# Kernel optimization log

Measured on AMD Instinct MI355X. Metric: run time of the kernel, lower is better.

The kernel has to match this reference:

```python
import jax, jax.numpy as jnp
import numpy as np

D = 300      # dim_in (hardcoded in HGConv)
N_CAT = 3    # n_categories
M = 16384    # nodes
E = 4096     # hyperedges


def setup_inputs() -> dict:
    key = jax.random.key(0)
    ks = jax.random.split(key, 11)
    s = 1.0 / np.sqrt(D)
    u = lambda k, shape: jax.random.uniform(k, shape, jnp.float32, -s, s)
    return {
        "node_feats": jax.random.normal(ks[0], (M, D), jnp.float32),
        "edge_feats": jax.random.normal(ks[1], (E, D), jnp.float32),
        "inc_mat": jax.random.uniform(ks[2], (M, E), jnp.float32),
        # VertexConv params (Linear weights stored as (in, out); torch stores transpose)
        "W_att": u(ks[3], (D, D)),       # attention, no bias
        "W_proj": u(ks[4], (D, D)),      # projection, no bias
        "alpha": jnp.array(0.5, jnp.float32),
        # HypergraphEdgeAggregation params
        "ec_W_att": u(ks[5], (D, 1)),    # attention, no bias
        "ec_W_proj": u(ks[6], (D, D)),
        "ec_b_proj": u(ks[7], (D,)),
        # final classifier
        "fc_W": u(ks[8], (D, N_CAT)),
        "fc_b": u(ks[9], (N_CAT,)),
    }


def reference(node_feats, edge_feats, inc_mat, W_att, W_proj, alpha,
              ec_W_att, ec_W_proj, ec_b_proj, fc_W, fc_b):
    # --- VertexConv ---
    # edge attention scores: inc^T @ (X @ W_att)  -> (e, d)
    edge_att = inc_mat.T @ (node_feats @ W_att)
    attn = jax.nn.softmax(edge_att, axis=1)
    # fused equivalent of einsum('me,md->med') then einsum('med,ed->ed'):
    # edge_feat[e,d] = (inc^T @ X)[e,d] * attn[e,d]
    ef = (inc_mat.T @ node_feats) * attn
    ef = ef @ W_proj
    ef = alpha * edge_feats + (1.0 - alpha) * ef          # residual mix
    # --- HypergraphEdgeAggregation ---
    scores = ef @ ec_W_att                                # (e, 1)
    w = jax.nn.softmax(scores, axis=0)                    # softmax over edges
    pooled = jnp.sum(ef * w, axis=0)                      # (d,)
    out = pooled @ ec_W_proj + ec_b_proj                  # (d,)
    # --- classifier (LogSoftmax is defined but NOT applied in forward) ---
    logits = out @ fc_W + fc_b                            # (n_categories,)
    return logits
```

## Files before the change

kernel.cpp:

```cpp
#include <hip/hip_runtime.h>
#include <math.h>

typedef _Float16 f16;
typedef _Float16 f16x8 __attribute__((ext_vector_type(8)));
typedef _Float16 f16x4 __attribute__((ext_vector_type(4)));
typedef __fp16 fp16x2 __attribute__((ext_vector_type(2)));
typedef float f32x4 __attribute__((ext_vector_type(4)));
typedef float f32x16 __attribute__((ext_vector_type(16)));

#define NM 16384
#define NE 4096
#define ND 300
#define DP 320
#define JT 640
#define PS 2621440

__device__ __forceinline__ int swz(int r) { return (r ^ (r >> 2)) & 3; }

#define GLOAD_LDS16(gsrc, ldst)                                              \
  __builtin_amdgcn_global_load_lds(                                          \
      (__attribute__((address_space(1))) void*)(gsrc),                       \
      (__attribute__((address_space(3))) void*)(ldst), 16, 0, 0)

__global__ void k0_wt(const float* __restrict__ Watt, f16* __restrict__ WT) {
  int idx = blockIdx.x * 256 + threadIdx.x;
  if (idx >= DP * DP) return;
  int j = idx / DP, d = idx % DP;
  float v = (j < ND && d < ND) ? Watt[d * ND + j] : 0.f;
  WT[(size_t)j * DP + d] = (f16)v;
}

__global__ __launch_bounds__(256) void k1a_xprep(const float* __restrict__ X,
                                                 f16* __restrict__ X16,
                                                 f16* __restrict__ YT) {
  __shared__ f16 tile[64][324];
  int m0 = blockIdx.x * 64;
  for (int idx = threadIdx.x; idx < 64 * 80; idx += 256) {
    int m = idx / 80, q = idx % 80;
    int d = q * 4;
    float4 v = make_float4(0.f, 0.f, 0.f, 0.f);
    if (d < ND) v = *(const float4*)(X + (size_t)(m0 + m) * ND + d);
    f16x4 hv;
    hv[0] = (f16)v.x; hv[1] = (f16)v.y; hv[2] = (f16)v.z; hv[3] = (f16)v.w;
    tile[m][d] = hv[0]; tile[m][d + 1] = hv[1];
    tile[m][d + 2] = hv[2]; tile[m][d + 3] = hv[3];
    *(f16x4*)(X16 + (size_t)(m0 + m) * DP + d) = hv;
  }
  __syncthreads();
  for (int idx = threadIdx.x; idx < DP * 8; idx += 256) {
    int d = idx >> 3, part = idx & 7;
    f16x8 hv;
#pragma unroll
    for (int i = 0; i < 8; ++i) hv[i] = tile[part * 8 + i][d];
    *(f16x8*)(YT + (size_t)(DP + d) * NM + m0 + part * 8) = hv;
  }
}

__global__ __launch_bounds__(512, 2) void k1b_xat(const f16* __restrict__ WT,
                                                  const f16* __restrict__ X16,
                                                  f16* __restrict__ YT) {
  __shared__ __align__(16) char lds[49152];
  const int t = threadIdx.x, lane = t & 63, wid = t >> 6;
  const int m0 = blockIdx.x * 64;
  const int row = lane & 15, g = lane >> 4;
  const int wj = wid & 3, wm = wid >> 2;
  int aoff[5], boff[2];
#pragma unroll
  for (int f = 0; f < 5; ++f) {
    int jr = wj * 80 + f * 16 + row;
    aoff[f] = jr * 64 + ((g ^ swz(jr)) << 4);
  }
#pragma unroll
  for (int fm = 0; fm < 2; ++fm) {
    int mr = wm * 32 + fm * 16 + row;
    boff[fm] = mr * 64 + ((g ^ swz(mr)) << 4);
  }
  f32x4 acc[5][2];
#pragma unroll
  for (int f = 0; f < 5; ++f)
#pragma unroll
    for (int fm = 0; fm < 2; ++fm)
#pragma unroll
      for (int r = 0; r < 4; ++r) acc[f][fm][r] = 0.f;

  auto stage = [&](int buf, int ks) {
    int k0 = ks * 32;
    char* A = lds + buf * 20480;
    char* B = lds + 40960 + buf * 4096;
    for (int c = wid; c < 24; c += 8) {
      if (c < 20) {
        int j = c * 16 + (lane >> 2), gg = lane & 3;
        GLOAD_LDS16(WT + (size_t)j * DP + k0 + 8 * (gg ^ swz(j)), A + c * 1024);
      } else {
        int cb = c - 20;
        int m = cb * 16 + (lane >> 2), gg = lane & 3;
        GLOAD_LDS16(X16 + (size_t)(m0 + m) * DP + k0 + 8 * (gg ^ swz(m)),
                    B + cb * 1024);
      }
    }
  };
  stage(0, 0);
  __syncthreads();
  for (int ks = 0; ks < 10; ++ks) {
    int cur = ks & 1;
    if (ks + 1 < 10) stage(cur ^ 1, ks + 1);
    const char* A = lds + cur * 20480;
    const char* B = lds + 40960 + cur * 4096;
    f16x8 b0 = *(const f16x8*)(B + boff[0]);
    f16x8 b1 = *(const f16x8*)(B + boff[1]);
#pragma unroll
    for (int f = 0; f < 5; ++f) {
      f16x8 a = *(const f16x8*)(A + aoff[f]);
      acc[f][0] = __builtin_amdgcn_mfma_f32_16x16x32_f16(a, b0, acc[f][0], 0, 0, 0);
      acc[f][1] = __builtin_amdgcn_mfma_f32_16x16x32_f16(a, b1, acc[f][1], 0, 0, 0);
    }
    __syncthreads();
  }
#pragma unroll
  for (int f = 0; f < 5; ++f)
#pragma unroll
    for (int fm = 0; fm < 2; ++fm)
#pragma unroll
      for (int r = 0; r < 4; ++r) {
        int j = wj * 80 + f * 16 + g * 4 + r;
        int m = m0 + wm * 32 + fm * 16 + row;
        YT[(size_t)j * NM + m] = (f16)acc[f][fm][r];
      }
}

#define K2WAIT(N) asm volatile("s_waitcnt vmcnt(" #N ") lgkmcnt(0)" ::: "memory")
#define K2BAR()                                        \
  do {                                                 \
    asm volatile("" ::: "memory");                     \
    __builtin_amdgcn_s_barrier();                      \
    asm volatile("" ::: "memory");                     \
  } while (0)

__global__ __launch_bounds__(256, 2) void k2_bigmm(const float* __restrict__ inc,
                                                   const f16* __restrict__ YT,
                                                   f16* __restrict__ Zp) {
  constexpr int STEPS = 64;
  __shared__ __align__(16) char lds[57344];
  const int t = threadIdx.x, lane = t & 63, wid = t >> 6;
  const int bx = blockIdx.x;
  const int kb = bx & 7, y = bx >> 3;
  const int eb = y & 31, jn = y >> 5;
  const int e0 = eb * 128, j0 = jn * 320;
  const size_t kbase = (size_t)kb * 2048;
  f16* __restrict__ Zout = Zp + (size_t)kb * PS;

  const int we = wid >> 1, wj = wid & 1;
  const int l31 = lane & 31, oct = lane >> 5;
  int sl[2];
#pragma unroll
  for (int kk = 0; kk < 2; ++kk)
    sl[kk] = (((kk * 2 + oct) ^ ((l31 >> 1) & 3)) & 3) << 4;
  const int arow = (we * 64 + l31) * 64;
  const int brow = (wj * 160 + l31) * 64;
  const int ep = t & 63, kq = t >> 6;
  const int sA = (kq ^ ((ep >> 1) & 3)) & 3;
  const int wa0 = 40960 + ep * 64 + sA * 16;
  const int wa1 = 40960 + (ep + 64) * 64 + sA * 16;
  const float* pA = inc + (kbase + kq * 8) * NE + e0 + ep;
  const int br = wid * 80 + (lane >> 2);
  const f16* pB = YT + (size_t)(j0 + br) * NM + kbase +
                  8 * ((lane & 3) ^ ((lane >> 3) & 3));

  float rAx[8], rAy[8], rBx[8], rBy[8];
  f32x16 acc[2][5];
#pragma unroll
  for (int me = 0; me < 2; ++me)
#pragma unroll
    for (int f = 0; f < 5; ++f)
#pragma unroll
      for (int r = 0; r < 16; ++r) acc[me][f][r] = 0.f;

#define LOADA(RX, RY)                                                          \
  {                                                                            \
    _Pragma("unroll") for (int i = 0; i < 8; ++i) {                            \
      RX[i] = pA[(size_t)i * NE];                                              \
      RY[i] = pA[(size_t)i * NE + 64];                                         \
    }                                                                          \
    pA += (size_t)32 * NE;                                                     \
  }
#define DMAB(S)                                                                \
  {                                                                            \
    _Pragma("unroll") for (int i = 0; i < 5; ++i) {                            \
      GLOAD_LDS16(pB + (size_t)(i * 16) * NM,                                  \
                  lds + (S)*20480 + wid * 5120 + i * 1024);                    \
    }                                                                          \
    pB += 32;                                                                  \
  }
#define WRITEA(RX, RY, S)                                                      \
  {                                                                            \
    union { fp16x2 h; uint32_t u; } ux_[4], uy_[4];                            \
    _Pragma("unroll") for (int z = 0; z < 4; ++z) {                            \
      ux_[z].h = __builtin_amdgcn_cvt_pkrtz(RX[2 * z], RX[2 * z + 1]);         \
      uy_[z].h = __builtin_amdgcn_cvt_pkrtz(RY[2 * z], RY[2 * z + 1]);         \
    }                                                                          \
    *(uint4*)(lds + wa0 + (S)*8192) =                                          \
        make_uint4(ux_[0].u, ux_[1].u, ux_[2].u, ux_[3].u);                    \
    *(uint4*)(lds + wa1 + (S)*8192) =                                          \
        make_uint4(uy_[0].u, uy_[1].u, uy_[2].u, uy_[3].u);                    \
  }
#define COMPUTE(S)                                                             \
  {                                                                            \
    __builtin_amdgcn_s_setprio(1);                                             \
    _Pragma("unroll") for (int kk = 0; kk < 2; ++kk) {                         \
      f16x8 a0_ = *(const f16x8*)(lds + 40960 + (S)*8192 + arow + sl[kk]);     \
      f16x8 a1_ = *(const f16x8*)(lds + 40960 + (S)*8192 + arow + 2048 + sl[kk]); \
      _Pragma("unroll") for (int f = 0; f < 5; ++f) {                          \
        f16x8 b_ = *(const f16x8*)(lds + (S)*20480 + brow + f * 2048 + sl[kk]); \
        acc[0][f] = __builtin_amdgcn_mfma_f32_32x32x16_f16(a0_, b_, acc[0][f], 0, 0, 0); \
        acc[1][f] = __builtin_amdgcn_mfma_f32_32x32x16_f16(a1_, b_, acc[1][f], 0, 0, 0); \
      }                                                                        \
    }                                                                          \
    __builtin_amdgcn_s_setprio(0);                                             \
  }

  LOADA(rAx, rAy);
  DMAB(0);
  WRITEA(rAx, rAy, 0);
  LOADA(rAx, rAy);
  DMAB(1);
  K2WAIT(21);
  K2BAR();

  for (int tt = 0; tt < STEPS - 2; ++tt) {
    COMPUTE(tt & 1);
    K2BAR();
    WRITEA(rAx, rAy, (tt + 1) & 1);
    LOADA(rAx, rAy);
    DMAB(tt & 1);
    K2WAIT(21);
    K2BAR();
  }
  COMPUTE(0);
  K2BAR();
  WRITEA(rAx, rAy, 1);
  K2WAIT(0);
  K2BAR();
  COMPUTE(1);

#pragma unroll
  for (int me = 0; me < 2; ++me)
#pragma unroll
    for (int f = 0; f < 5; ++f) {
      int jg = j0 + wj * 160 + f * 32 + l31;
      int ebase = e0 + we * 64 + me * 32 + 4 * oct;
#pragma unroll
      for (int r = 0; r < 16; ++r) {
        int eg = ebase + (r & 3) + 8 * (r >> 2);
        Zout[(size_t)eg * JT + jg] = (f16)acc[me][f][r];
      }
    }
#undef LOADA
#undef DMAB
#undef WRITEA
#undef COMPUTE
}

__global__ __launch_bounds__(256) void k3_edge(const f16* __restrict__ Zp,
                                               const float* __restrict__ edge_feats,
                                               const float* __restrict__ Wproj,
                                               const float* __restrict__ alphaP,
                                               const float* __restrict__ ecWatt,
                                               float* __restrict__ ef,
                                               float* __restrict__ scores) {
  __shared__ float efw[16][304];
  const int t = threadIdx.x, lane = t & 63, w = t >> 6;
  const int e0 = blockIdx.x * 16;
  for (int el = 0; el < 4; ++el) {
    int e = e0 + w * 4 + el;
    const size_t ro = (size_t)e * JT;
    float p[5];
    float mx = -1e30f;
#pragma unroll
    for (int u = 0; u < 5; ++u) {
      int d = u * 64 + lane;
      float zv = -1e30f;
      if (d < ND) {
        zv = 0.f;
#pragma unroll
        for (int i = 0; i < 8; ++i) zv += (float)Zp[(size_t)i * PS + ro + d];
      }
      p[u] = zv;
      mx = fmaxf(mx, p[u]);
    }
    for (int o = 32; o; o >>= 1) mx = fmaxf(mx, __shfl_xor(mx, o));
    float s = 0.f;
#pragma unroll
    for (int u = 0; u < 5; ++u) {
      int d = u * 64 + lane;
      float pe = (d < ND) ? expf(p[u] - mx) : 0.f;
      p[u] = pe;
      s += pe;
    }
    for (int o = 32; o; o >>= 1) s += __shfl_xor(s, o);
    float inv = 1.f / s;
#pragma unroll
    for (int u = 0; u < 5; ++u) {
      int d = u * 64 + lane;
      if (d < 304) {
        float rv = 0.f;
        if (d < ND) {
#pragma unroll
          for (int i = 0; i < 8; ++i) rv += (float)Zp[(size_t)i * PS + ro + DP + d];
          rv *= p[u] * inv;
        }
        efw[w * 4 + el][d] = rv;
      }
    }
  }
  __syncthreads();
  const int jl = lane & 15, kc = lane >> 4;
  const float alpha = alphaP[0];
  float acc[4][19];
#pragma unroll
  for (int ei = 0; ei < 4; ++ei)
#pragma unroll
    for (int jj = 0; jj < 19; ++jj) acc[ei][jj] = 0.f;
  const int d0 = kc * 75;
  const float* efw0 = &efw[w * 4 + 0][0];
  const float* efw1 = &efw[w * 4 + 1][0];
  const float* efw2 = &efw[w * 4 + 2][0];
  const float* efw3 = &efw[w * 4 + 3][0];
  for (int dd = 0; dd < 75; ++dd) {
    int d = d0 + dd;
    const float* wr = Wproj + (size_t)d * ND + jl;
    float w0 = efw0[d], w1 = efw1[d], w2 = efw2[d], w3 = efw3[d];
#pragma unroll
    for (int jj = 0; jj < 19; ++jj) {
      int j = jl + jj * 16;
      float wv = (j < ND) ? wr[jj * 16] : 0.f;
      acc[0][jj] += w0 * wv;
      acc[1][jj] += w1 * wv;
      acc[2][jj] += w2 * wv;
      acc[3][jj] += w3 * wv;
    }
  }
#pragma unroll
  for (int ei = 0; ei < 4; ++ei)
#pragma unroll
    for (int jj = 0; jj < 19; ++jj) {
      acc[ei][jj] += __shfl_xor(acc[ei][jj], 16);
      acc[ei][jj] += __shfl_xor(acc[ei][jj], 32);
    }
  float scp[4] = {0.f, 0.f, 0.f, 0.f};
#pragma unroll
  for (int ei = 0; ei < 4; ++ei) {
    int e = e0 + w * 4 + ei;
#pragma unroll
    for (int jj = 0; jj < 19; ++jj) {
      int j = jl + jj * 16;
      float v = 0.f;
      if (j < ND) {
        v = alpha * edge_feats[(size_t)e * ND + j] + (1.f - alpha) * acc[ei][jj];
        scp[ei] += v * ecWatt[j];
      }
      if (kc == 0) ef[(size_t)e * 304 + j] = v;
    }
  }
#pragma unroll
  for (int ei = 0; ei < 4; ++ei)
    for (int o = 8; o; o >>= 1) scp[ei] += __shfl_xor(scp[ei], o);
  if (lane == 0) {
#pragma unroll
    for (int ei = 0; ei < 4; ++ei) scores[e0 + w * 4 + ei] = scp[ei];
  }
}

__global__ __launch_bounds__(1024) void k4a_softmax(const float* __restrict__ scores,
                                                    float* __restrict__ w) {
  __shared__ float red[16];
  __shared__ float red2[16];
  const int t = threadIdx.x, lane = t & 63, wv = t >> 6;
  float v[4];
  float mx = -1e30f;
#pragma unroll
  for (int u = 0; u < 4; ++u) {
    v[u] = scores[t + u * 1024];
    mx = fmaxf(mx, v[u]);
  }
  for (int o = 32; o; o >>= 1) mx = fmaxf(mx, __shfl_xor(mx, o));
  if (lane == 0) red[wv] = mx;
  __syncthreads();
  float m2 = red[0];
  for (int i = 1; i < 16; ++i) m2 = fmaxf(m2, red[i]);
  float s = 0.f;
#pragma unroll
  for (int u = 0; u < 4; ++u) {
    v[u] = expf(v[u] - m2);
    s += v[u];
  }
  for (int o = 32; o; o >>= 1) s += __shfl_xor(s, o);
  if (lane == 0) red2[wv] = s;
  __syncthreads();
  float S = 0.f;
  for (int i = 0; i < 16; ++i) S += red2[i];
  float inv = 1.f / S;
#pragma unroll
  for (int u = 0; u < 4; ++u) w[t + u * 1024] = v[u] * inv;
}

__global__ __launch_bounds__(256) void k4b_pool(const float* __restrict__ ef,
                                                const float* __restrict__ w,
                                                float* __restrict__ partial) {
  const int b = blockIdx.x, t = threadIdx.x;
  const int e0 = b * 64;
  for (int j = t; j < 304; j += 256) {
    float acc = 0.f;
    for (int e = 0; e < 64; ++e) acc += w[e0 + e] * ef[(size_t)(e0 + e) * 304 + j];
    partial[b * 304 + j] = acc;
  }
}

__global__ __launch_bounds__(256) void k4c_final(const float* __restrict__ partial,
                                                 const float* __restrict__ ecWp,
                                                 const float* __restrict__ ecb,
                                                 const float* __restrict__ fcW,
                                                 const float* __restrict__ fcb,
                                                 float* __restrict__ out) {
  __shared__ float pooled[304];
  __shared__ float o[304];
  const int t = threadIdx.x;
  for (int j = t; j < 304; j += 256) {
    float acc = 0.f;
    for (int b = 0; b < 64; ++b) acc += partial[b * 304 + j];
    pooled[j] = acc;
  }
  __syncthreads();
  for (int j2 = t; j2 < ND; j2 += 256) {
    float acc = ecb[j2];
    for (int j = 0; j < ND; ++j) acc += pooled[j] * ecWp[j * ND + j2];
    o[j2] = acc;
  }
  __syncthreads();
  if (t < 3) {
    float acc = fcb[t];
    for (int j2 = 0; j2 < ND; ++j2) acc += o[j2] * fcW[j2 * 3 + t];
    out[t] = acc;
  }
}

extern "C" void kernel_launch(void* const* d_in, const int* in_sizes, int n_in,
                              void* d_out, int out_size, void* d_ws, size_t ws_size,
                              hipStream_t stream) {
  const float* X = (const float*)d_in[0];
  const float* EF = (const float*)d_in[1];
  const float* INC = (const float*)d_in[2];
  const float* WATT = (const float*)d_in[3];
  const float* WPROJ = (const float*)d_in[4];
  const float* ALPHA = (const float*)d_in[5];
  const float* ECATT = (const float*)d_in[6];
  const float* ECWP = (const float*)d_in[7];
  const float* ECB = (const float*)d_in[8];
  const float* FCW = (const float*)d_in[9];
  const float* FCB = (const float*)d_in[10];

  char* ws = (char*)d_ws;
  f16* YT = (f16*)(ws);
  f16* X16 = (f16*)(ws + 20971520);
  f16* Zp = (f16*)(ws + 20971520);
  f16* WT = (f16*)(ws + 62914560);
  float* ef = (float*)(ws + 63119360);
  float* sc = (float*)(ws + 68100096);
  float* wv = (float*)(ws + 68116480);
  float* pp = (float*)(ws + 68132864);

  hipLaunchKernelGGL(k0_wt, dim3(400), dim3(256), 0, stream, WATT, WT);
  hipLaunchKernelGGL(k1a_xprep, dim3(256), dim3(256), 0, stream, X, X16, YT);
  hipLaunchKernelGGL(k1b_xat, dim3(256), dim3(512), 0, stream, WT, X16, YT);
  hipLaunchKernelGGL(k2_bigmm, dim3(512), dim3(256), 0, stream, INC, YT, Zp);
  hipLaunchKernelGGL(k3_edge, dim3(256), dim3(256), 0, stream, Zp, EF, WPROJ,
                     ALPHA, ECATT, ef, sc);
  hipLaunchKernelGGL(k4a_softmax, dim3(1), dim3(1024), 0, stream, sc, wv);
  hipLaunchKernelGGL(k4b_pool, dim3(64), dim3(256), 0, stream, ef, wv, pp);
  hipLaunchKernelGGL(k4c_final, dim3(1), dim3(256), 0, stream, pp, ECWP, ECB, FCW,
                     FCB, (float*)d_out);
}
```

Before: 293.8 us.

## Reassociate attention matmul to apply W_att after the incidence reduction

The old path computed X@W_att over all nodes and concatenated it with X, so the big incidence GEMM had twice the output width (640 columns). The new path uses inc^T@(X@W_att) = (inc^T@X)@W_att: the big GEMM only runs over X (320 columns), with split-K widened to 16 partitions. A new reduction kernel sums the partials into a half-precision edge matrix, and a small MFMA GEMM applies W_att per edge. This roughly halves the dominant GEMM's work and drops the node-level X@W_att kernel, at the cost of two extra launches and a half-precision rounding of inc^T@X before the attention projection.

```diff
diff --git a/kernel.cpp b/kernel.cpp
--- a/kernel.cpp
+++ b/kernel.cpp
@@ -12,8 +12,7 @@
 #define NE 4096
 #define ND 300
 #define DP 320
-#define JT 640
-#define PS 2621440
+#define PS 1310720
 
 __device__ __forceinline__ int swz(int r) { return (r ^ (r >> 2)) & 3; }
 
@@ -31,8 +30,7 @@
 }
 
 __global__ __launch_bounds__(256) void k1a_xprep(const float* __restrict__ X,
-                                                 f16* __restrict__ X16,
-                                                 f16* __restrict__ YT) {
+                                                 f16* __restrict__ XT) {
   __shared__ f16 tile[64][324];
   int m0 = blockIdx.x * 64;
   for (int idx = threadIdx.x; idx < 64 * 80; idx += 256) {
@@ -40,11 +38,8 @@
     int d = q * 4;
     float4 v = make_float4(0.f, 0.f, 0.f, 0.f);
     if (d < ND) v = *(const float4*)(X + (size_t)(m0 + m) * ND + d);
-    f16x4 hv;
-    hv[0] = (f16)v.x; hv[1] = (f16)v.y; hv[2] = (f16)v.z; hv[3] = (f16)v.w;
-    tile[m][d] = hv[0]; tile[m][d + 1] = hv[1];
-    tile[m][d + 2] = hv[2]; tile[m][d + 3] = hv[3];
-    *(f16x4*)(X16 + (size_t)(m0 + m) * DP + d) = hv;
+    tile[m][d] = (f16)v.x; tile[m][d + 1] = (f16)v.y;
+    tile[m][d + 2] = (f16)v.z; tile[m][d + 3] = (f16)v.w;
   }
   __syncthreads();
   for (int idx = threadIdx.x; idx < DP * 8; idx += 256) {
@@ -52,80 +47,8 @@
     f16x8 hv;
 #pragma unroll
     for (int i = 0; i < 8; ++i) hv[i] = tile[part * 8 + i][d];
-    *(f16x8*)(YT + (size_t)(DP + d) * NM + m0 + part * 8) = hv;
-  }
-}
-
-__global__ __launch_bounds__(512, 2) void k1b_xat(const f16* __restrict__ WT,
-                                                  const f16* __restrict__ X16,
-                                                  f16* __restrict__ YT) {
-  __shared__ __align__(16) char lds[49152];
-  const int t = threadIdx.x, lane = t & 63, wid = t >> 6;
-  const int m0 = blockIdx.x * 64;
-  const int row = lane & 15, g = lane >> 4;
-  const int wj = wid & 3, wm = wid >> 2;
-  int aoff[5], boff[2];
-#pragma unroll
-  for (int f = 0; f < 5; ++f) {
-    int jr = wj * 80 + f * 16 + row;
-    aoff[f] = jr * 64 + ((g ^ swz(jr)) << 4);
-  }
-#pragma unroll
-  for (int fm = 0; fm < 2; ++fm) {
-    int mr = wm * 32 + fm * 16 + row;
-    boff[fm] = mr * 64 + ((g ^ swz(mr)) << 4);
-  }
-  f32x4 acc[5][2];
-#pragma unroll
-  for (int f = 0; f < 5; ++f)
-#pragma unroll
-    for (int fm = 0; fm < 2; ++fm)
-#pragma unroll
-      for (int r = 0; r < 4; ++r) acc[f][fm][r] = 0.f;
-
-  auto stage = [&](int buf, int ks) {
-    int k0 = ks * 32;
-    char* A = lds + buf * 20480;
-    char* B = lds + 40960 + buf * 4096;
-    for (int c = wid; c < 24; c += 8) {
-      if (c < 20) {
-        int j = c * 16 + (lane >> 2), gg = lane & 3;
-        GLOAD_LDS16(WT + (size_t)j * DP + k0 + 8 * (gg ^ swz(j)), A + c * 1024);
-      } else {
-        int cb = c - 20;
-        int m = cb * 16 + (lane >> 2), gg = lane & 3;
-        GLOAD_LDS16(X16 + (size_t)(m0 + m) * DP + k0 + 8 * (gg ^ swz(m)),
-                    B + cb * 1024);
-      }
-    }
-  };
-  stage(0, 0);
-  __syncthreads();
-  for (int ks = 0; ks < 10; ++ks) {
-    int cur = ks & 1;
-    if (ks + 1 < 10) stage(cur ^ 1, ks + 1);
-    const char* A = lds + cur * 20480;
-    const char* B = lds + 40960 + cur * 4096;
-    f16x8 b0 = *(const f16x8*)(B + boff[0]);
-    f16x8 b1 = *(const f16x8*)(B + boff[1]);
-#pragma unroll
-    for (int f = 0; f < 5; ++f) {
-      f16x8 a = *(const f16x8*)(A + aoff[f]);
-      acc[f][0] = __builtin_amdgcn_mfma_f32_16x16x32_f16(a, b0, acc[f][0], 0, 0, 0);
-      acc[f][1] = __builtin_amdgcn_mfma_f32_16x16x32_f16(a, b1, acc[f][1], 0, 0, 0);
-    }
-    __syncthreads();
-  }
-#pragma unroll
-  for (int f = 0; f < 5; ++f)
-#pragma unroll
-    for (int fm = 0; fm < 2; ++fm)
-#pragma unroll
-      for (int r = 0; r < 4; ++r) {
-        int j = wj * 80 + f * 16 + g * 4 + r;
-        int m = m0 + wm * 32 + fm * 16 + row;
-        YT[(size_t)j * NM + m] = (f16)acc[f][fm][r];
-      }
+    *(f16x8*)(XT + (size_t)d * NM + m0 + part * 8) = hv;
+  }
 }
 
 #define K2WAIT(N) asm volatile("s_waitcnt vmcnt(" #N ") lgkmcnt(0)" ::: "memory")
@@ -137,16 +60,16 @@
   } while (0)
 
 __global__ __launch_bounds__(256, 2) void k2_bigmm(const float* __restrict__ inc,
-                                                   const f16* __restrict__ YT,
+                                                   const f16* __restrict__ XT,
                                                    f16* __restrict__ Zp) {
-  constexpr int STEPS = 64;
+  constexpr int STEPS = 32;
   __shared__ __align__(16) char lds[57344];
   const int t = threadIdx.x, lane = t & 63, wid = t >> 6;
   const int bx = blockIdx.x;
-  const int kb = bx & 7, y = bx >> 3;
-  const int eb = y & 31, jn = y >> 5;
-  const int e0 = eb * 128, j0 = jn * 320;
-  const size_t kbase = (size_t)kb * 2048;
+  const int kb = (bx & 7) | (((bx >> 3) & 1) << 3);
+  const int eb = bx >> 4;
+  const int e0 = eb * 128;
+  const size_t kbase = (size_t)kb * 1024;
   f16* __restrict__ Zout = Zp + (size_t)kb * PS;
 
   const int we = wid >> 1, wj = wid & 1;
@@ -163,10 +86,9 @@
   const int wa1 = 40960 + (ep + 64) * 64 + sA * 16;
   const float* pA = inc + (kbase + kq * 8) * NE + e0 + ep;
   const int br = wid * 80 + (lane >> 2);
-  const f16* pB = YT + (size_t)(j0 + br) * NM + kbase +
-                  8 * ((lane & 3) ^ ((lane >> 3) & 3));
-
-  float rAx[8], rAy[8], rBx[8], rBy[8];
+  const f16* pB = XT + (size_t)br * NM + kbase + 8 * ((lane & 3) ^ ((lane >> 3) & 3));
+
+  float rAx[8], rAy[8];
   f32x16 acc[2][5];
 #pragma unroll
   for (int me = 0; me < 2; ++me)
@@ -246,21 +168,108 @@
   for (int me = 0; me < 2; ++me)
 #pragma unroll
     for (int f = 0; f < 5; ++f) {
-      int jg = j0 + wj * 160 + f * 32 + l31;
+      int jg = wj * 160 + f * 32 + l31;
       int ebase = e0 + we * 64 + me * 32 + 4 * oct;
 #pragma unroll
       for (int r = 0; r < 16; ++r) {
         int eg = ebase + (r & 3) + 8 * (r >> 2);
-        Zout[(size_t)eg * JT + jg] = (f16)acc[me][f][r];
+        Zout[(size_t)eg * DP + jg] = (f16)acc[me][f][r];
       }
     }
 #undef LOADA
 #undef DMAB
 #undef WRITEA
+}
+
+__global__ __launch_bounds__(256) void k2s_sum(const f16* __restrict__ Zp,
+                                               f16* __restrict__ EF0) {
+  const int idx = (blockIdx.x * 256 + threadIdx.x) * 4;
+  float s0 = 0.f, s1 = 0.f, s2 = 0.f, s3 = 0.f;
+#pragma unroll
+  for (int i = 0; i < 16; ++i) {
+    f16x4 v = *(const f16x4*)(Zp + (size_t)i * PS + idx);
+    s0 += (float)v[0]; s1 += (float)v[1]; s2 += (float)v[2]; s3 += (float)v[3];
+  }
+  f16x4 o;
+  o[0] = (f16)s0; o[1] = (f16)s1; o[2] = (f16)s2; o[3] = (f16)s3;
+  *(f16x4*)(EF0 + idx) = o;
+}
+
+__global__ __launch_bounds__(256, 1) void k2b_att(const f16* __restrict__ EF0,
+                                                  const f16* __restrict__ WT,
+                                                  float* __restrict__ att) {
+  constexpr int STEPS = 10;
+  __shared__ __align__(16) char lds[57344];
+  const int t = threadIdx.x, lane = t & 63, wid = t >> 6;
+  const int e0 = blockIdx.x * 128;
+  const int we = wid >> 1, wj = wid & 1;
+  const int l31 = lane & 31, oct = lane >> 5;
+  int sl[2];
+#pragma unroll
+  for (int kk = 0; kk < 2; ++kk)
+    sl[kk] = (((kk * 2 + oct) ^ ((l31 >> 1) & 3)) & 3) << 4;
+  const int arow = (we * 64 + l31) * 64;
+  const int brow = (wj * 160 + l31) * 64;
+  const int srcsw = 8 * ((lane & 3) ^ ((lane >> 3) & 3));
+  const f16* pA = EF0 + (size_t)(e0 + wid * 32 + (lane >> 2)) * DP + srcsw;
+  const f16* pB = WT + (size_t)(wid * 80 + (lane >> 2)) * DP + srcsw;
+
+  f32x16 acc[2][5];
+#pragma unroll
+  for (int me = 0; me < 2; ++me)
+#pragma unroll
+    for (int f = 0; f < 5; ++f)
+#pragma unroll
+      for (int r = 0; r < 16; ++r) acc[me][f][r] = 0.f;
+
+#define STAGE2(S)                                                              \
+  {                                                                            \
+    _Pragma("unroll") for (int i = 0; i < 2; ++i) {                            \
+      GLOAD_LDS16(pA + (size_t)(i * 16) * DP,                                  \
+                  lds + 40960 + (S)*8192 + wid * 2048 + i * 1024);             \
+    }                                                                          \
+    pA += 32;                                                                  \
+    _Pragma("unroll") for (int i = 0; i < 5; ++i) {                            \
+      GLOAD_LDS16(pB + (size_t)(i * 16) * DP,                                  \
+                  lds + (S)*20480 + wid * 5120 + i * 1024);                    \
+    }                                                                          \
+    pB += 32;                                                                  \
+  }
+
+  STAGE2(0);
+  STAGE2(1);
+  K2WAIT(7);
+  K2BAR();
+  for (int tt = 0; tt < STEPS - 2; ++tt) {
+    COMPUTE(tt & 1);
+    K2BAR();
+    STAGE2(tt & 1);
+    K2WAIT(7);
+    K2BAR();
+  }
+  COMPUTE(0);
+  K2BAR();
+  K2WAIT(0);
+  COMPUTE(1);
+
+#pragma unroll
+  for (int me = 0; me < 2; ++me)
+#pragma unroll
+    for (int f = 0; f < 5; ++f) {
+      int jg = wj * 160 + f * 32 + l31;
+      int ebase = e0 + we * 64 + me * 32 + 4 * oct;
+#pragma unroll
+      for (int r = 0; r < 16; ++r) {
+        int eg = ebase + (r & 3) + 8 * (r >> 2);
+        att[(size_t)eg * DP + jg] = acc[me][f][r];
+      }
+    }
+#undef STAGE2
 #undef COMPUTE
 }
 
-__global__ __launch_bounds__(256) void k3_edge(const f16* __restrict__ Zp,
+__global__ __launch_bounds__(256) void k3_edge(const float* __restrict__ att,
+                                               const f16* __restrict__ EF0,
                                                const float* __restrict__ edge_feats,
                                                const float* __restrict__ Wproj,
                                                const float* __restrict__ alphaP,
@@ -272,19 +281,13 @@
   const int e0 = blockIdx.x * 16;
   for (int el = 0; el < 4; ++el) {
     int e = e0 + w * 4 + el;
-    const size_t ro = (size_t)e * JT;
+    const size_t ro = (size_t)e * DP;
     float p[5];
     float mx = -1e30f;
 #pragma unroll
     for (int u = 0; u < 5; ++u) {
       int d = u * 64 + lane;
-      float zv = -1e30f;
-      if (d < ND) {
-        zv = 0.f;
-#pragma unroll
-        for (int i = 0; i < 8; ++i) zv += (float)Zp[(size_t)i * PS + ro + d];
-      }
-      p[u] = zv;
+      p[u] = (d < ND) ? att[ro + d] : -1e30f;
       mx = fmaxf(mx, p[u]);
     }
     for (int o = 32; o; o >>= 1) mx = fmaxf(mx, __shfl_xor(mx, o));
@@ -301,15 +304,8 @@
 #pragma unroll
     for (int u = 0; u < 5; ++u) {
       int d = u * 64 + lane;
-      if (d < 304) {
-        float rv = 0.f;
-        if (d < ND) {
-#pragma unroll
-          for (int i = 0; i < 8; ++i) rv += (float)Zp[(size_t)i * PS + ro + DP + d];
-          rv *= p[u] * inv;
-        }
-        efw[w * 4 + el][d] = rv;
-      }
+      if (d < 304)
+        efw[w * 4 + el][d] = (d < ND) ? (float)EF0[ro + d] * p[u] * inv : 0.f;
     }
   }
   __syncthreads();
@@ -447,7 +443,7 @@
                               void* d_out, int out_size, void* d_ws, size_t ws_size,
                               hipStream_t stream) {
   const float* X = (const float*)d_in[0];
-  const float* EF = (const float*)d_in[1];
+  const float* EFEATS = (const float*)d_in[1];
   const float* INC = (const float*)d_in[2];
   const float* WATT = (const float*)d_in[3];
   const float* WPROJ = (const float*)d_in[4];
@@ -459,21 +455,23 @@
   const float* FCB = (const float*)d_in[10];
 
   char* ws = (char*)d_ws;
-  f16* YT = (f16*)(ws);
-  f16* X16 = (f16*)(ws + 20971520);
-  f16* Zp = (f16*)(ws + 20971520);
-  f16* WT = (f16*)(ws + 62914560);
-  float* ef = (float*)(ws + 63119360);
-  float* sc = (float*)(ws + 68100096);
-  float* wv = (float*)(ws + 68116480);
-  float* pp = (float*)(ws + 68132864);
+  f16* XT = (f16*)(ws);
+  f16* Zp = (f16*)(ws + 10485760);
+  f16* WT = (f16*)(ws + 52428800);
+  f16* EF0 = (f16*)(ws + 52633600);
+  float* att = (float*)(ws + 55255040);
+  float* ef = (float*)(ws + 60497920);
+  float* sc = (float*)(ws + 65478656);
+  float* wv = (float*)(ws + 65495040);
+  float* pp = (float*)(ws + 65511424);
 
   hipLaunchKernelGGL(k0_wt, dim3(400), dim3(256), 0, stream, WATT, WT);
-  hipLaunchKernelGGL(k1a_xprep, dim3(256), dim3(256), 0, stream, X, X16, YT);
-  hipLaunchKernelGGL(k1b_xat, dim3(256), dim3(512), 0, stream, WT, X16, YT);
-  hipLaunchKernelGGL(k2_bigmm, dim3(512), dim3(256), 0, stream, INC, YT, Zp);
-  hipLaunchKernelGGL(k3_edge, dim3(256), dim3(256), 0, stream, Zp, EF, WPROJ,
-                     ALPHA, ECATT, ef, sc);
+  hipLaunchKernelGGL(k1a_xprep, dim3(256), dim3(256), 0, stream, X, XT);
+  hipLaunchKernelGGL(k2_bigmm, dim3(512), dim3(256), 0, stream, INC, XT, Zp);
+  hipLaunchKernelGGL(k2s_sum, dim3(1280), dim3(256), 0, stream, Zp, EF0);
+  hipLaunchKernelGGL(k2b_att, dim3(32), dim3(256), 0, stream, EF0, WT, att);
+  hipLaunchKernelGGL(k3_edge, dim3(256), dim3(256), 0, stream, att, EF0, EFEATS,
+                     WPROJ, ALPHA, ECATT, ef, sc);
   hipLaunchKernelGGL(k4a_softmax, dim3(1), dim3(1024), 0, stream, sc, wv);
   hipLaunchKernelGGL(k4b_pool, dim3(64), dim3(256), 0, stream, ef, wv, pp);
   hipLaunchKernelGGL(k4c_final, dim3(1), dim3(256), 0, stream, pp, ECWP, ECB, FCW,
```

Result: faster. 252.1 us (-14.2%).
